# Kernel tuning notes

Measured on AMD Instinct MI355X. Metric: run time of the kernel, lower is better.

The kernel has to match this reference:

```python
import jax, jax.numpy as jnp
import numpy as np

N = 10000; E = 160000; NF = 5; EF = 3; H = 8; C = 128; HC = H * C; G = 16

def _glorot(key, shape):
    s = float(np.sqrt(6.0 / (shape[0] + shape[-1])))
    return jax.random.uniform(key, shape, minval=-s, maxval=s, dtype=jnp.float32)

def setup_inputs():
    key = jax.random.key(0)
    ks = jax.random.split(key, 32)
    inp = {}
    inp["x"] = jax.random.normal(ks[0], (N, NF), dtype=jnp.float32)
    inp["edge_index"] = jax.random.randint(ks[1], (2, E), 0, N, dtype=jnp.int32)
    inp["edge_attr"] = jax.random.normal(ks[2], (E, EF), dtype=jnp.float32)
    inp["batch"] = jnp.sort(jax.random.randint(ks[3], (N,), 0, G, dtype=jnp.int32))
    ins = [NF, HC, HC, HC]
    i = 4
    for l in range(4):
        inp[f"W{l+1}"] = _glorot(ks[i], (ins[l], HC)); i += 1
        inp[f"We{l+1}"] = _glorot(ks[i], (EF, HC)); i += 1
        inp[f"as{l+1}"] = _glorot(ks[i], (H, C)); i += 1
        inp[f"ad{l+1}"] = _glorot(ks[i], (H, C)); i += 1
        inp[f"ae{l+1}"] = _glorot(ks[i], (H, C)); i += 1
        inp[f"b{l+1}"] = jnp.zeros((HC if l < 3 else C,), jnp.float32)
    inp["lin_w"] = _glorot(ks[i], (C, 1)) * 2.0
    inp["lin_b"] = jnp.zeros((1,), jnp.float32)
    return inp

def _gat(x, src, dst, ea, W, We, a_s, a_d, a_e, bias, concat):
    # PyG GATConv with edge_dim, add_self_loops=True, fill_value='mean'
    n = x.shape[0]
    cnt = jax.ops.segment_sum(jnp.ones((src.shape[0],), x.dtype), dst, n)
    loop_attr = jax.ops.segment_sum(ea, dst, n) / jnp.maximum(cnt, 1.0)[:, None]
    sl = jnp.arange(n, dtype=src.dtype)
    src2 = jnp.concatenate([src, sl])
    dst2 = jnp.concatenate([dst, sl])
    ea2 = jnp.concatenate([ea, loop_attr], axis=0)
    xl = (x @ W).reshape(n, H, C)                       # [N,H,C]
    a_src = jnp.einsum("nhc,hc->nh", xl, a_s)
    a_dst = jnp.einsum("nhc,hc->nh", xl, a_d)
    el = (ea2 @ We).reshape(-1, H, C)                    # [E2,H,C]
    alpha = a_src[src2] + a_dst[dst2] + jnp.einsum("ehc,hc->eh", el, a_e)
    alpha = jax.nn.leaky_relu(alpha, 0.2)
    m = jax.ops.segment_max(alpha, dst2, n)
    m = jnp.where(jnp.isfinite(m), m, 0.0)
    ex = jnp.exp(alpha - m[dst2])
    den = jax.ops.segment_sum(ex, dst2, n)
    alpha = ex / (den[dst2] + 1e-16)                     # segment softmax over dst
    out = jax.ops.segment_sum(alpha[:, :, None] * xl[src2], dst2, n)  # [N,H,C]
    if concat:
        return out.reshape(n, HC) + bias
    return out.mean(axis=1) + bias

def reference(x, edge_index, edge_attr, batch,
              W1, We1, as1, ad1, ae1, b1,
              W2, We2, as2, ad2, ae2, b2,
              W3, We3, as3, ad3, ae3, b3,
              W4, We4, as4, ad4, ae4, b4,
              lin_w, lin_b):
    src, dst = edge_index[0], edge_index[1]
    h = jax.nn.elu(_gat(x, src, dst, edge_attr, W1, We1, as1, ad1, ae1, b1, True))
    h = jax.nn.elu(_gat(h, src, dst, edge_attr, W2, We2, as2, ad2, ae2, b2, True))
    h = jax.nn.elu(_gat(h, src, dst, edge_attr, W3, We3, as3, ad3, ae3, b3, True))
    h = jax.nn.elu(_gat(h, src, dst, edge_attr, W4, We4, as4, ad4, ae4, b4, False))
    cnt = jax.ops.segment_sum(jnp.ones((N,), h.dtype), batch, G)
    pooled = jax.ops.segment_sum(h, batch, G) / jnp.maximum(cnt, 1.0)[:, None]
    return (pooled @ lin_w + lin_b).squeeze(-1)
```

## Files before the change

### kernel.cpp

```cpp
#include <hip/hip_runtime.h>
#include <math.h>

#define Nn 10000
#define En 160000
#define NF 5
#define EF 3
#define Hh 8
#define Cc 128
#define HC 1024
#define Gg 16

#define Mpad 10112

typedef __attribute__((ext_vector_type(8))) _Float16 half8;
typedef __attribute__((ext_vector_type(4))) float f32x4;


__device__ __forceinline__ void gl_lds16(const void* g, void* l) {
    __builtin_amdgcn_global_load_lds((const __attribute__((address_space(1))) void*)g,
                                     (__attribute__((address_space(3))) void*)l, 16, 0, 0);
}

__device__ __forceinline__ float elu_f(float v) {
    return (v > 0.f) ? v : expm1f(v);
}


__global__ void deg_sum_k(const int* __restrict__ dst, int* __restrict__ cnt) {
    int e = blockIdx.x * 256 + threadIdx.x;
    if (e >= En) return;
    atomicAdd(&cnt[dst[e]], 1);
}

__global__ __launch_bounds__(1024) void scan_k(const int* __restrict__ cnt,
                                               int* __restrict__ rowptr,
                                               int* __restrict__ fillptr,
                                               const int* __restrict__ batch,
                                               int* __restrict__ gstart) {
    __shared__ int sh[1024];
    int tid = threadIdx.x;
    int base = tid * 10;
    int loc[10];
    int tsum = 0;
#pragma unroll
    for (int j = 0; j < 10; ++j) {
        int i = base + j;
        int v = (i < Nn) ? cnt[i] : 0;
        loc[j] = tsum;
        tsum += v;
    }
    sh[tid] = tsum;
    __syncthreads();
    for (int off = 1; off < 1024; off <<= 1) {
        int t = (tid >= off) ? sh[tid - off] : 0;
        __syncthreads();
        sh[tid] += t;
        __syncthreads();
    }
    int excl = sh[tid] - tsum;
#pragma unroll
    for (int j = 0; j < 10; ++j) {
        int i = base + j;
        if (i < Nn) {
            rowptr[i] = excl + loc[j];
            fillptr[i] = excl + loc[j];
        }
    }
    if (tid == 1023) rowptr[Nn] = sh[1023];
#pragma unroll
    for (int j = 0; j < 10; ++j) {
        int i = base + j;
        if (i < Nn) {
            int b = batch[i];
            if (i == 0) {
                for (int g = 0; g <= b; ++g) gstart[g] = 0;
            } else {
                int pb = batch[i - 1];
                for (int g = pb + 1; g <= b; ++g) gstart[g] = i;
            }
            if (i == Nn - 1) {
                for (int g = b + 1; g <= Gg; ++g) gstart[g] = Nn;
            }
        }
    }
}

__global__ void csr_fill_k(const int* __restrict__ src, const int* __restrict__ dst,
                           const float* __restrict__ ea, int* __restrict__ fillptr,
                           float4* __restrict__ eaP, float* __restrict__ loop_attr) {
    int e = blockIdx.x * 256 + threadIdx.x;
    if (e >= En) return;
    int d = dst[e];
    float e0 = ea[e * 3 + 0], e1 = ea[e * 3 + 1], e2 = ea[e * 3 + 2];
    int pos = atomicAdd(&fillptr[d], 1);
    eaP[pos] = make_float4(e0, e1, e2, __int_as_float(src[e]));
    atomicAdd(&loop_attr[d * 3 + 0], e0);
    atomicAdd(&loop_attr[d * 3 + 1], e1);
    atomicAdd(&loop_attr[d * 3 + 2], e2);
}


__global__ void wae_all_k(const float* __restrict__ We1, const float* __restrict__ ae1,
                          const float* __restrict__ We2, const float* __restrict__ ae2,
                          const float* __restrict__ We3, const float* __restrict__ ae3,
                          const float* __restrict__ We4, const float* __restrict__ ae4,
                          float* __restrict__ w_ae_all) {
    int t = threadIdx.x;
    if (t >= 96) return;
    int l = t / 24, idx = t % 24;
    int f = idx >> 3, h = idx & 7;
    const float* We = (l == 0) ? We1 : (l == 1) ? We2 : (l == 2) ? We3 : We4;
    const float* ae = (l == 0) ? ae1 : (l == 1) ? ae2 : (l == 2) ? ae3 : ae4;
    float s = 0.f;
    for (int c = 0; c < Cc; ++c) s += We[f * HC + h * Cc + c] * ae[h * Cc + c];
    w_ae_all[l * 24 + f * 8 + h] = s;
}

__global__ __launch_bounds__(1024) void wsplit_all_k(const float* __restrict__ W2,
                                                     const float* __restrict__ W3,
                                                     const float* __restrict__ W4,
                                                     _Float16* __restrict__ Wt16) {
    __shared__ float tile[32][33];
    int z = blockIdx.z;
    const float* W = (z == 0) ? W2 : (z == 1) ? W3 : W4;
    int nb = blockIdx.x * 32, kb = blockIdx.y * 32;
    tile[threadIdx.y][threadIdx.x] = W[(size_t)(kb + threadIdx.y) * HC + nb + threadIdx.x];
    __syncthreads();
    float x = tile[threadIdx.x][threadIdx.y];
    int n = nb + threadIdx.y, k = kb + threadIdx.x;
    Wt16[(size_t)z * HC * HC + (size_t)n * HC + k] = (_Float16)x;
}


__global__ void gemm_k5(const float* __restrict__ x, const float* __restrict__ Wm,
                        const float* __restrict__ a_s, const float* __restrict__ a_d,
                        _Float16* __restrict__ out16,
                        float* __restrict__ a_srcB, float* __restrict__ a_dstB) {
    int n = blockIdx.x;
    int tid = threadIdx.x;
    __shared__ float xr[8];
    __shared__ float vrow[HC];
    if (tid < NF) xr[tid] = x[n * NF + tid];
    __syncthreads();
    float x0 = xr[0], x1 = xr[1], x2 = xr[2], x3 = xr[3], x4 = xr[4];
    for (int j = tid; j < HC; j += 256) {
        float v = x0 * Wm[j] + x1 * Wm[HC + j] + x2 * Wm[2 * HC + j]
                + x3 * Wm[3 * HC + j] + x4 * Wm[4 * HC + j];
        out16[(size_t)n * HC + j] = (_Float16)v;
        vrow[j] = v;
    }
    __syncthreads();
    int w = tid >> 6, lane = tid & 63;
#pragma unroll
    for (int q = 0; q < 2; ++q) {
        int h = w * 2 + q;
        float v0 = vrow[h * Cc + lane], v1 = vrow[h * Cc + 64 + lane];
        float s1 = v0 * a_s[h * Cc + lane] + v1 * a_s[h * Cc + 64 + lane];
        float s2 = v0 * a_d[h * Cc + lane] + v1 * a_d[h * Cc + 64 + lane];
#pragma unroll
        for (int off = 32; off; off >>= 1) {
            s1 += __shfl_xor(s1, off);
            s2 += __shfl_xor(s2, off);
        }
        if (lane == 0) { a_srcB[n * 8 + h] = s1; a_dstB[n * 8 + h] = s2; }
    }
}

__global__ __launch_bounds__(256) void gemm_mfma(const _Float16* __restrict__ A,
                                                 const _Float16* __restrict__ Bt,
                                                 const float* __restrict__ a_s,
                                                 const float* __restrict__ a_d,
                                                 _Float16* __restrict__ C16,
                                                 float* __restrict__ a_srcB,
                                                 float* __restrict__ a_dstB) {
    __shared__ _Float16 As[128 * 32];
    __shared__ _Float16 Bs[128 * 32];
    __shared__ float ps[128][2];
    __shared__ float pd[128][2];
    int tid = threadIdx.x;
    int wave = tid >> 6, lane = tid & 63;
    int wr = wave >> 1, wc = wave & 1;
    int row0 = blockIdx.y * 128;
    int col0 = blockIdx.x * 128;
    int h = blockIdx.x;

    f32x4 acc[4][4];
#pragma unroll
    for (int i = 0; i < 4; ++i)
#pragma unroll
        for (int j = 0; j < 4; ++j) acc[i][j] = (f32x4){0.f, 0.f, 0.f, 0.f};

    int srow = lane >> 2;
    int scol = (lane & 3) * 8;
    int fr = lane & 15;
    int fk = (lane >> 4) * 8;

    for (int kb = 0; kb < 1024; kb += 32) {
#pragma unroll
        for (int cc = 0; cc < 2; ++cc) {
            int c = wave + cc * 4;
            int r = c * 16 + srow;
            gl_lds16(A + (size_t)(row0 + r) * 1024 + kb + scol, &As[c * 512 + lane * 8]);
            gl_lds16(Bt + (size_t)(col0 + r) * 1024 + kb + scol, &Bs[c * 512 + lane * 8]);
        }
        __syncthreads();

        half8 af[4], bf[4];
#pragma unroll
        for (int i = 0; i < 4; ++i)
            af[i] = *(const half8*)&As[(wr * 64 + i * 16 + fr) * 32 + fk];
#pragma unroll
        for (int j = 0; j < 4; ++j)
            bf[j] = *(const half8*)&Bs[(wc * 64 + j * 16 + fr) * 32 + fk];
#pragma unroll
        for (int i = 0; i < 4; ++i)
#pragma unroll
            for (int j = 0; j < 4; ++j)
                acc[i][j] = __builtin_amdgcn_mfma_f32_16x16x32_f16(af[i], bf[j], acc[i][j],
                                                                   0, 0, 0);
        __syncthreads();
    }

    int cn = lane & 15, rq = (lane >> 4) * 4;
#pragma unroll
    for (int i = 0; i < 4; ++i) {
        int rbase = row0 + wr * 64 + i * 16 + rq;
#pragma unroll
        for (int j = 0; j < 4; ++j) {
            int col = col0 + wc * 64 + j * 16 + cn;
#pragma unroll
            for (int r = 0; r < 4; ++r) {
                int row = rbase + r;
                if (row < Nn) C16[(size_t)row * HC + col] = (_Float16)acc[i][j][r];
            }
        }
    }
    float asv[4], adv[4];
#pragma unroll
    for (int j = 0; j < 4; ++j) {
        int c = wc * 64 + j * 16 + cn;
        asv[j] = a_s[h * Cc + c];
        adv[j] = a_d[h * Cc + c];
    }
#pragma unroll
    for (int i = 0; i < 4; ++i)
#pragma unroll
        for (int r = 0; r < 4; ++r) {
            float rs = acc[i][0][r] * asv[0] + acc[i][1][r] * asv[1]
                     + acc[i][2][r] * asv[2] + acc[i][3][r] * asv[3];
            float rd = acc[i][0][r] * adv[0] + acc[i][1][r] * adv[1]
                     + acc[i][2][r] * adv[2] + acc[i][3][r] * adv[3];
#pragma unroll
            for (int off = 1; off < 16; off <<= 1) {
                rs += __shfl_xor(rs, off);
                rd += __shfl_xor(rd, off);
            }
            if (cn == 0) {
                int rib = wr * 64 + i * 16 + rq + r;
                ps[rib][wc] = rs;
                pd[rib][wc] = rd;
            }
        }
    __syncthreads();
    if (tid < 128) {
        int row = row0 + tid;
        if (row < Nn) {
            a_srcB[row * 8 + h] = ps[tid][0] + ps[tid][1];
            a_dstB[row * 8 + h] = pd[tid][0] + pd[tid][1];
        }
    }
}


__global__ __launch_bounds__(256, 4) void aggregate_k(const _Float16* __restrict__ xl16,
                                                      const float4* __restrict__ eaP,
                                                      const float* __restrict__ loop_attr,
                                                      const float* __restrict__ a_srcB,
                                                      const float* __restrict__ a_dstB,
                                                      const float* __restrict__ w_ae,
                                                      const int* __restrict__ rowptr,
                                                      const float* __restrict__ bias,
                                                      const float* __restrict__ lin_w,
                                                      _Float16* __restrict__ A2,
                                                      float* __restrict__ dnode,
                                                      int raw_mode) {
    int lane = threadIdx.x & 63;
    int n = blockIdx.x * 4 + (threadIdx.x >> 6);
    if (n >= Nn) return;
    int beg = rowptr[n], end = rowptr[n + 1];
    int hc = lane >> 3;

    float w0c = w_ae[hc], w1c = w_ae[8 + hc], w2c = w_ae[16 + hc];
    float adst_n = a_dstB[n * 8 + hc];
    float asrc_n = a_srcB[n * 8 + hc];
    float invd = 1.0f / fmaxf((float)(end - beg), 1.0f);
    float f0 = loop_attr[n * 3 + 0] * invd;
    float f1 = loop_attr[n * 3 + 1] * invd;
    float f2 = loop_attr[n * 3 + 2] * invd;
    float av = asrc_n + adst_n + f0 * w0c + f1 * w1c + f2 * w2c;
    float aself = (av > 0.f) ? av : 0.2f * av;

    int loff = lane * 16;

    const _Float16* rp = xl16 + (size_t)n * HC + loff;
    half8 r0 = *(const half8*)rp;
    half8 r1 = *(const half8*)(rp + 8);
    float acc[16];
#pragma unroll
    for (int j = 0; j < 8; ++j) {
        acc[j] = (float)r0[j];
        acc[8 + j] = (float)r1[j];
    }
    float s = 1.0f;

    for (int i0 = beg; i0 < end; i0 += 4) {
        bool v1 = (i0 + 1 < end), v2 = (i0 + 2 < end), v3 = (i0 + 3 < end);
        int i1 = v1 ? i0 + 1 : i0;
        int i2 = v2 ? i0 + 2 : i0;
        int i3 = v3 ? i0 + 3 : i0;
        float4 e0 = eaP[i0], e1 = eaP[i1], e2 = eaP[i2], e3 = eaP[i3];
        int s0 = __float_as_int(e0.w), s1 = __float_as_int(e1.w);
        int s2 = __float_as_int(e2.w), s3 = __float_as_int(e3.w);
        float as0 = a_srcB[s0 * 8 + hc], as1 = a_srcB[s1 * 8 + hc];
        float as2 = a_srcB[s2 * 8 + hc], as3 = a_srcB[s3 * 8 + hc];
        const _Float16* p0 = xl16 + (size_t)s0 * HC + loff;
        const _Float16* p1 = xl16 + (size_t)s1 * HC + loff;
        const _Float16* p2 = xl16 + (size_t)s2 * HC + loff;
        const _Float16* p3 = xl16 + (size_t)s3 * HC + loff;
        half8 q0a = *(const half8*)p0, q0b = *(const half8*)(p0 + 8);
        half8 q1a = *(const half8*)p1, q1b = *(const half8*)(p1 + 8);
        half8 q2a = *(const half8*)p2, q2b = *(const half8*)(p2 + 8);
        half8 q3a = *(const half8*)p3, q3b = *(const half8*)(p3 + 8);
        float al0 = as0 + adst_n + e0.x * w0c + e0.y * w1c + e0.z * w2c;
        float al1 = as1 + adst_n + e1.x * w0c + e1.y * w1c + e1.z * w2c;
        float al2 = as2 + adst_n + e2.x * w0c + e2.y * w1c + e2.z * w2c;
        float al3 = as3 + adst_n + e3.x * w0c + e3.y * w1c + e3.z * w2c;
        al0 = (al0 > 0.f) ? al0 : 0.2f * al0;
        al1 = (al1 > 0.f) ? al1 : 0.2f * al1;
        al2 = (al2 > 0.f) ? al2 : 0.2f * al2;
        al3 = (al3 > 0.f) ? al3 : 0.2f * al3;
        float u0 = __expf(al0 - aself);
        float u1 = v1 ? __expf(al1 - aself) : 0.f;
        float u2 = v2 ? __expf(al2 - aself) : 0.f;
        float u3 = v3 ? __expf(al3 - aself) : 0.f;
        s += u0 + u1 + u2 + u3;
#pragma unroll
        for (int j = 0; j < 8; ++j) {
            float t0 = acc[j], t1 = acc[8 + j];
            t0 = fmaf(u0, (float)q0a[j], t0);  t1 = fmaf(u0, (float)q0b[j], t1);
            t0 = fmaf(u1, (float)q1a[j], t0);  t1 = fmaf(u1, (float)q1b[j], t1);
            t0 = fmaf(u2, (float)q2a[j], t0);  t1 = fmaf(u2, (float)q2b[j], t1);
            t0 = fmaf(u3, (float)q3a[j], t0);  t1 = fmaf(u3, (float)q3b[j], t1);
            acc[j] = t0; acc[8 + j] = t1;
        }
    }

    float inv = 1.f / (s + 1e-16f);

    if (!raw_mode) {
        int ch = loff;
        half8 hv0, hv1;
#pragma unroll
        for (int j = 0; j < 8; ++j) {
            hv0[j] = (_Float16)elu_f(fmaf(acc[j], inv, bias[ch + j]));
            hv1[j] = (_Float16)elu_f(fmaf(acc[8 + j], inv, bias[ch + 8 + j]));
        }
        _Float16* p = A2 + (size_t)n * 1024 + ch;
        *(half8*)p = hv0;
        *(half8*)(p + 8) = hv1;
    } else {
#pragma unroll
        for (int j = 0; j < 16; ++j) acc[j] *= inv;
#pragma unroll
        for (int off = 8; off < 64; off <<= 1)
#pragma unroll
            for (int j = 0; j < 16; ++j) acc[j] += __shfl_xor(acc[j], off);
        int c0 = (lane & 7) * 16;
        float partial = 0.f;
#pragma unroll
        for (int j = 0; j < 16; ++j) {
            float v = elu_f(acc[j] * 0.125f + bias[c0 + j]);
            partial = fmaf(v, lin_w[c0 + j], partial);
        }
#pragma unroll
        for (int off = 1; off < 8; off <<= 1) partial += __shfl_xor(partial, off);
        if (lane == 0) dnode[n] = partial;
    }
}


__global__ __launch_bounds__(256) void pool_final_k(const float* __restrict__ dnode,
                                                    const int* __restrict__ gstart,
                                                    const float* __restrict__ lin_b,
                                                    float* __restrict__ out) {
    __shared__ float sh[256];
    int g = blockIdx.x;
    int tid = threadIdx.x;
    int s = gstart[g], e = gstart[g + 1];
    float acc = 0.f;
    for (int n = s + tid; n < e; n += 256) acc += dnode[n];
    sh[tid] = acc;
    __syncthreads();
    for (int off = 128; off; off >>= 1) {
        if (tid < off) sh[tid] += sh[tid + off];
        __syncthreads();
    }
    if (tid == 0) out[g] = sh[0] / fmaxf((float)(e - s), 1.f) + lin_b[0];
}


extern "C" void kernel_launch(void* const* d_in, const int* in_sizes, int n_in,
                              void* d_out, int out_size, void* d_ws, size_t ws_size,
                              hipStream_t stream) {
    const float* x = (const float*)d_in[0];
    const int* ei = (const int*)d_in[1];
    const float* ea = (const float*)d_in[2];
    const int* batch = (const int*)d_in[3];
    const float *Wl[4], *Wel[4], *asl[4], *adl[4], *ael[4], *bl[4];
    for (int l = 0; l < 4; ++l) {
        Wl[l] = (const float*)d_in[4 + 6 * l];
        Wel[l] = (const float*)d_in[5 + 6 * l];
        asl[l] = (const float*)d_in[6 + 6 * l];
        adl[l] = (const float*)d_in[7 + 6 * l];
        ael[l] = (const float*)d_in[8 + 6 * l];
        bl[l] = (const float*)d_in[9 + 6 * l];
    }
    const float* lin_w = (const float*)d_in[28];
    const float* lin_b = (const float*)d_in[29];
    const int* srcA = ei;
    const int* dstA = ei + En;

    float* Wp = (float*)d_ws;
    size_t o = 0;
    _Float16* A2 = (_Float16*)(Wp + o); o += (size_t)Mpad * 512;
    _Float16* Wt16 = (_Float16*)(Wp + o); o += (size_t)3 * HC * HC / 2;
    _Float16* xl16 = (_Float16*)(Wp + o); o += (size_t)Nn * HC / 2;
    float4* eaP = (float4*)(Wp + o); o += (size_t)En * 4;
    float* loop_attr = Wp + o; o += Nn * 3;
    int* cnt = (int*)(Wp + o); o += Nn;
    int* rowptr = (int*)(Wp + o); o += Nn + 1;
    int* fillptr = (int*)(Wp + o); o += Nn;
    int* gstart = (int*)(Wp + o); o += Gg + 1;
    float* a_srcB = Wp + o; o += Nn * Hh;
    float* a_dstB = Wp + o; o += Nn * Hh;
    float* w_ae_all = Wp + o; o += 128;
    float* dnode = Wp + o; o += Nn;

    hipMemsetAsync(cnt, 0, Nn * sizeof(int), stream);
    hipMemsetAsync(loop_attr, 0, Nn * 3 * sizeof(float), stream);

    deg_sum_k<<<(En + 255) / 256, 256, 0, stream>>>(dstA, cnt);
    scan_k<<<1, 1024, 0, stream>>>(cnt, rowptr, fillptr, batch, gstart);
    csr_fill_k<<<(En + 255) / 256, 256, 0, stream>>>(srcA, dstA, ea, fillptr, eaP,
                                                     loop_attr);
    wae_all_k<<<1, 128, 0, stream>>>(Wel[0], ael[0], Wel[1], ael[1], Wel[2], ael[2],
                                     Wel[3], ael[3], w_ae_all);
    wsplit_all_k<<<dim3(32, 32, 3), dim3(32, 32), 0, stream>>>(Wl[1], Wl[2], Wl[3], Wt16);

    for (int l = 0; l < 4; ++l) {
        if (l == 0)
            gemm_k5<<<Nn, 256, 0, stream>>>(x, Wl[0], asl[0], adl[0], xl16, a_srcB, a_dstB);
        else
            gemm_mfma<<<dim3(HC / 128, Mpad / 128), 256, 0, stream>>>(
                A2, Wt16 + (size_t)(l - 1) * HC * HC, asl[l], adl[l], xl16, a_srcB, a_dstB);
        aggregate_k<<<(Nn + 3) / 4, 256, 0, stream>>>(xl16, eaP, loop_attr, a_srcB,
                                                      a_dstB, w_ae_all + l * 24, rowptr,
                                                      bl[l], lin_w, A2, dnode,
                                                      (l == 3) ? 1 : 0);
    }
    pool_final_k<<<Gg, 256, 0, stream>>>(dnode, gstart, lin_b, (float*)d_out);
}
```

Measured before the change: 572.0 us.

## Split each node's edge aggregation across two waves and broadcast edge data via readlane

The aggregation kernel now assigns two wavefronts per destination node. Each wave processes half of the node's incoming edges, and the partial accumulators and softmax sums are combined through shared memory. Edge source indices and attributes are loaded coalesced, one per lane, in chunks of 64 and then broadcast with readlane, which replaces the per-edge uniform loads. This raises parallelism and memory-level concurrency per node. The cost is an extra srcIdx array, a block-level barrier, and LDS traffic for the combine.

New measurement: 546.1 us. -4.5%, faster.

```diff
diff --git a/kernel.cpp b/kernel.cpp
--- a/kernel.cpp
+++ b/kernel.cpp
@@ -23,6 +23,10 @@
 
 __device__ __forceinline__ float elu_f(float v) {
     return (v > 0.f) ? v : expm1f(v);
+}
+
+__device__ __forceinline__ float rl_f(float v, int k) {
+    return __int_as_float(__builtin_amdgcn_readlane(__float_as_int(v), k));
 }
 
 
@@ -87,13 +91,16 @@
 
 __global__ void csr_fill_k(const int* __restrict__ src, const int* __restrict__ dst,
                            const float* __restrict__ ea, int* __restrict__ fillptr,
-                           float4* __restrict__ eaP, float* __restrict__ loop_attr) {
+                           float4* __restrict__ eaP, int* __restrict__ srcIdxW,
+                           float* __restrict__ loop_attr) {
     int e = blockIdx.x * 256 + threadIdx.x;
     if (e >= En) return;
     int d = dst[e];
     float e0 = ea[e * 3 + 0], e1 = ea[e * 3 + 1], e2 = ea[e * 3 + 2];
+    int sv = src[e];
     int pos = atomicAdd(&fillptr[d], 1);
-    eaP[pos] = make_float4(e0, e1, e2, __int_as_float(src[e]));
+    eaP[pos] = make_float4(e0, e1, e2, __int_as_float(sv));
+    srcIdxW[pos] = sv;
     atomicAdd(&loop_attr[d * 3 + 0], e0);
     atomicAdd(&loop_attr[d * 3 + 1], e1);
     atomicAdd(&loop_attr[d * 3 + 2], e2);
@@ -274,6 +281,7 @@
 
 __global__ __launch_bounds__(256, 4) void aggregate_k(const _Float16* __restrict__ xl16,
                                                       const float4* __restrict__ eaP,
+                                                      const int* __restrict__ srcIdx,
                                                       const float* __restrict__ loop_attr,
                                                       const float* __restrict__ a_srcB,
                                                       const float* __restrict__ a_dstB,
@@ -284,77 +292,126 @@
                                                       _Float16* __restrict__ A2,
                                                       float* __restrict__ dnode,
                                                       int raw_mode) {
-    int lane = threadIdx.x & 63;
-    int n = blockIdx.x * 4 + (threadIdx.x >> 6);
-    if (n >= Nn) return;
-    int beg = rowptr[n], end = rowptr[n + 1];
+    __shared__ float cmbA[2][4][256];
+    __shared__ float cmbS[2][64];
+    int tid = threadIdx.x;
+    int lane = tid & 63;
+    int wav = tid >> 6;
+    int local = wav >> 1;
+    int sub = __builtin_amdgcn_readfirstlane(wav & 1);
+    int n = __builtin_amdgcn_readfirstlane(blockIdx.x * 2 + local);
+    int beg = __builtin_amdgcn_readfirstlane(rowptr[n]);
+    int end = __builtin_amdgcn_readfirstlane(rowptr[n + 1]);
+    int deg = end - beg;
     int hc = lane >> 3;
 
     float w0c = w_ae[hc], w1c = w_ae[8 + hc], w2c = w_ae[16 + hc];
     float adst_n = a_dstB[n * 8 + hc];
     float asrc_n = a_srcB[n * 8 + hc];
-    float invd = 1.0f / fmaxf((float)(end - beg), 1.0f);
+    float invd = 1.0f / fmaxf((float)deg, 1.0f);
     float f0 = loop_attr[n * 3 + 0] * invd;
     float f1 = loop_attr[n * 3 + 1] * invd;
     float f2 = loop_attr[n * 3 + 2] * invd;
     float av = asrc_n + adst_n + f0 * w0c + f1 * w1c + f2 * w2c;
     float aself = (av > 0.f) ? av : 0.2f * av;
 
+    int hw = (deg + 1) >> 1;
+    int myBeg = beg + sub * hw;
+    int myEnd = sub ? end : beg + hw;
+
     int loff = lane * 16;
-
-    const _Float16* rp = xl16 + (size_t)n * HC + loff;
-    half8 r0 = *(const half8*)rp;
-    half8 r1 = *(const half8*)(rp + 8);
     float acc[16];
-#pragma unroll
-    for (int j = 0; j < 8; ++j) {
-        acc[j] = (float)r0[j];
-        acc[8 + j] = (float)r1[j];
-    }
-    float s = 1.0f;
-
-    for (int i0 = beg; i0 < end; i0 += 4) {
-        bool v1 = (i0 + 1 < end), v2 = (i0 + 2 < end), v3 = (i0 + 3 < end);
-        int i1 = v1 ? i0 + 1 : i0;
-        int i2 = v2 ? i0 + 2 : i0;
-        int i3 = v3 ? i0 + 3 : i0;
-        float4 e0 = eaP[i0], e1 = eaP[i1], e2 = eaP[i2], e3 = eaP[i3];
-        int s0 = __float_as_int(e0.w), s1 = __float_as_int(e1.w);
-        int s2 = __float_as_int(e2.w), s3 = __float_as_int(e3.w);
-        float as0 = a_srcB[s0 * 8 + hc], as1 = a_srcB[s1 * 8 + hc];
-        float as2 = a_srcB[s2 * 8 + hc], as3 = a_srcB[s3 * 8 + hc];
-        const _Float16* p0 = xl16 + (size_t)s0 * HC + loff;
-        const _Float16* p1 = xl16 + (size_t)s1 * HC + loff;
-        const _Float16* p2 = xl16 + (size_t)s2 * HC + loff;
-        const _Float16* p3 = xl16 + (size_t)s3 * HC + loff;
-        half8 q0a = *(const half8*)p0, q0b = *(const half8*)(p0 + 8);
-        half8 q1a = *(const half8*)p1, q1b = *(const half8*)(p1 + 8);
-        half8 q2a = *(const half8*)p2, q2b = *(const half8*)(p2 + 8);
-        half8 q3a = *(const half8*)p3, q3b = *(const half8*)(p3 + 8);
-        float al0 = as0 + adst_n + e0.x * w0c + e0.y * w1c + e0.z * w2c;
-        float al1 = as1 + adst_n + e1.x * w0c + e1.y * w1c + e1.z * w2c;
-        float al2 = as2 + adst_n + e2.x * w0c + e2.y * w1c + e2.z * w2c;
-        float al3 = as3 + adst_n + e3.x * w0c + e3.y * w1c + e3.z * w2c;
-        al0 = (al0 > 0.f) ? al0 : 0.2f * al0;
-        al1 = (al1 > 0.f) ? al1 : 0.2f * al1;
-        al2 = (al2 > 0.f) ? al2 : 0.2f * al2;
-        al3 = (al3 > 0.f) ? al3 : 0.2f * al3;
-        float u0 = __expf(al0 - aself);
-        float u1 = v1 ? __expf(al1 - aself) : 0.f;
-        float u2 = v2 ? __expf(al2 - aself) : 0.f;
-        float u3 = v3 ? __expf(al3 - aself) : 0.f;
-        s += u0 + u1 + u2 + u3;
+    float s;
+    if (sub == 0) {
+        const _Float16* rp = xl16 + (size_t)n * HC + loff;
+        half8 r0 = *(const half8*)rp;
+        half8 r1 = *(const half8*)(rp + 8);
 #pragma unroll
         for (int j = 0; j < 8; ++j) {
-            float t0 = acc[j], t1 = acc[8 + j];
-            t0 = fmaf(u0, (float)q0a[j], t0);  t1 = fmaf(u0, (float)q0b[j], t1);
-            t0 = fmaf(u1, (float)q1a[j], t0);  t1 = fmaf(u1, (float)q1b[j], t1);
-            t0 = fmaf(u2, (float)q2a[j], t0);  t1 = fmaf(u2, (float)q2b[j], t1);
-            t0 = fmaf(u3, (float)q3a[j], t0);  t1 = fmaf(u3, (float)q3b[j], t1);
-            acc[j] = t0; acc[8 + j] = t1;
-        }
-    }
-
+            acc[j] = (float)r0[j];
+            acc[8 + j] = (float)r1[j];
+        }
+        s = 1.0f;
+    } else {
+#pragma unroll
+        for (int j = 0; j < 16; ++j) acc[j] = 0.f;
+        s = 0.0f;
+    }
+
+    for (int base = myBeg; base < myEnd; base += 64) {
+        int cnt = myEnd - base;
+        if (cnt > 64) cnt = 64;
+        int li = base + ((lane < cnt) ? lane : 0);
+        int src_l = srcIdx[li];
+        float4 e_l = eaP[li];
+        for (int k = 0; k < cnt; k += 4) {
+            int k1 = (k + 1 < cnt) ? k + 1 : k;
+            int k2 = (k + 2 < cnt) ? k + 2 : k;
+            int k3 = (k + 3 < cnt) ? k + 3 : k;
+            bool v1 = (k + 1 < cnt), v2 = (k + 2 < cnt), v3 = (k + 3 < cnt);
+            int s0 = __builtin_amdgcn_readlane(src_l, k);
+            int s1 = __builtin_amdgcn_readlane(src_l, k1);
+            int s2 = __builtin_amdgcn_readlane(src_l, k2);
+            int s3 = __builtin_amdgcn_readlane(src_l, k3);
+            float e0x = rl_f(e_l.x, k),  e0y = rl_f(e_l.y, k),  e0z = rl_f(e_l.z, k);
+            float e1x = rl_f(e_l.x, k1), e1y = rl_f(e_l.y, k1), e1z = rl_f(e_l.z, k1);
+            float e2x = rl_f(e_l.x, k2), e2y = rl_f(e_l.y, k2), e2z = rl_f(e_l.z, k2);
+            float e3x = rl_f(e_l.x, k3), e3y = rl_f(e_l.y, k3), e3z = rl_f(e_l.z, k3);
+            float as0 = a_srcB[s0 * 8 + hc], as1 = a_srcB[s1 * 8 + hc];
+            float as2 = a_srcB[s2 * 8 + hc], as3 = a_srcB[s3 * 8 + hc];
+            const _Float16* p0 = xl16 + (size_t)s0 * HC + loff;
+            const _Float16* p1 = xl16 + (size_t)s1 * HC + loff;
+            const _Float16* p2 = xl16 + (size_t)s2 * HC + loff;
+            const _Float16* p3 = xl16 + (size_t)s3 * HC + loff;
+            half8 q0a = *(const half8*)p0, q0b = *(const half8*)(p0 + 8);
+            half8 q1a = *(const half8*)p1, q1b = *(const half8*)(p1 + 8);
+            half8 q2a = *(const half8*)p2, q2b = *(const half8*)(p2 + 8);
+            half8 q3a = *(const half8*)p3, q3b = *(const half8*)(p3 + 8);
+            float al0 = as0 + adst_n + e0x * w0c + e0y * w1c + e0z * w2c;
+            float al1 = as1 + adst_n + e1x * w0c + e1y * w1c + e1z * w2c;
+            float al2 = as2 + adst_n + e2x * w0c + e2y * w1c + e2z * w2c;
+            float al3 = as3 + adst_n + e3x * w0c + e3y * w1c + e3z * w2c;
+            al0 = (al0 > 0.f) ? al0 : 0.2f * al0;
+            al1 = (al1 > 0.f) ? al1 : 0.2f * al1;
+            al2 = (al2 > 0.f) ? al2 : 0.2f * al2;
+            al3 = (al3 > 0.f) ? al3 : 0.2f * al3;
+            float u0 = __expf(al0 - aself);
+            float u1 = v1 ? __expf(al1 - aself) : 0.f;
+            float u2 = v2 ? __expf(al2 - aself) : 0.f;
+            float u3 = v3 ? __expf(al3 - aself) : 0.f;
+            s += u0 + u1 + u2 + u3;
+#pragma unroll
+            for (int j = 0; j < 8; ++j) {
+                float t0 = acc[j], t1 = acc[8 + j];
+                t0 = fmaf(u0, (float)q0a[j], t0);  t1 = fmaf(u0, (float)q0b[j], t1);
+                t0 = fmaf(u1, (float)q1a[j], t0);  t1 = fmaf(u1, (float)q1b[j], t1);
+                t0 = fmaf(u2, (float)q2a[j], t0);  t1 = fmaf(u2, (float)q2b[j], t1);
+                t0 = fmaf(u3, (float)q3a[j], t0);  t1 = fmaf(u3, (float)q3b[j], t1);
+                acc[j] = t0; acc[8 + j] = t1;
+            }
+        }
+    }
+
+    if (sub == 1) {
+#pragma unroll
+        for (int j4 = 0; j4 < 4; ++j4)
+            *(float4*)&cmbA[local][j4][lane * 4] =
+                make_float4(acc[j4 * 4 + 0], acc[j4 * 4 + 1],
+                            acc[j4 * 4 + 2], acc[j4 * 4 + 3]);
+        cmbS[local][lane] = s;
+    }
+    __syncthreads();
+    if (sub == 1) return;
+
+    s += cmbS[local][lane];
+#pragma unroll
+    for (int j4 = 0; j4 < 4; ++j4) {
+        float4 c4 = *(const float4*)&cmbA[local][j4][lane * 4];
+        acc[j4 * 4 + 0] += c4.x;
+        acc[j4 * 4 + 1] += c4.y;
+        acc[j4 * 4 + 2] += c4.z;
+        acc[j4 * 4 + 3] += c4.w;
+    }
     float inv = 1.f / (s + 1e-16f);
 
     if (!raw_mode) {
@@ -436,6 +493,7 @@
     _Float16* Wt16 = (_Float16*)(Wp + o); o += (size_t)3 * HC * HC / 2;
     _Float16* xl16 = (_Float16*)(Wp + o); o += (size_t)Nn * HC / 2;
     float4* eaP = (float4*)(Wp + o); o += (size_t)En * 4;
+    int* srcIdx = (int*)(Wp + o); o += En;
     float* loop_attr = Wp + o; o += Nn * 3;
     int* cnt = (int*)(Wp + o); o += Nn;
     int* rowptr = (int*)(Wp + o); o += Nn + 1;
@@ -452,7 +510,7 @@
     deg_sum_k<<<(En + 255) / 256, 256, 0, stream>>>(dstA, cnt);
     scan_k<<<1, 1024, 0, stream>>>(cnt, rowptr, fillptr, batch, gstart);
     csr_fill_k<<<(En + 255) / 256, 256, 0, stream>>>(srcA, dstA, ea, fillptr, eaP,
-                                                     loop_attr);
+                                                     srcIdx, loop_attr);
     wae_all_k<<<1, 128, 0, stream>>>(Wel[0], ael[0], Wel[1], ael[1], Wel[2], ael[2],
                                      Wel[3], ael[3], w_ae_all);
     wsplit_all_k<<<dim3(32, 32, 3), dim3(32, 32), 0, stream>>>(Wl[1], Wl[2], Wl[3], Wt16);
@@ -463,10 +521,10 @@
         else
             gemm_mfma<<<dim3(HC / 128, Mpad / 128), 256, 0, stream>>>(
                 A2, Wt16 + (size_t)(l - 1) * HC * HC, asl[l], adl[l], xl16, a_srcB, a_dstB);
-        aggregate_k<<<(Nn + 3) / 4, 256, 0, stream>>>(xl16, eaP, loop_attr, a_srcB,
-                                                      a_dstB, w_ae_all + l * 24, rowptr,
-                                                      bl[l], lin_w, A2, dnode,
-                                                      (l == 3) ? 1 : 0);
+        aggregate_k<<<Nn / 2, 256, 0, stream>>>(xl16, eaP, srcIdx, loop_attr, a_srcB,
+                                                a_dstB, w_ae_all + l * 24, rowptr,
+                                                bl[l], lin_w, A2, dnode,
+                                                (l == 3) ? 1 : 0);
     }
     pool_final_k<<<Gg, 256, 0, stream>>>(dnode, gstart, lin_b, (float*)d_out);
 }
```
